# Kernel optimization log

Hardware: AMD Instinct MI355X
Metric: run time of the kernel (lower is better)

The kernel has to match this reference:

```python
import jax, jax.numpy as jnp
import numpy as np

N_VALUES = 10
STRIDE = 2

# sign binarization with straight-through estimator (identity gradient)
@jax.custom_vjp
def binarize(x):
    return jnp.sign(x)

def _bin_fwd(x):
    return jnp.sign(x), None

def _bin_bwd(res, g):
    return (g,)

binarize.defvjp(_bin_fwd, _bin_bwd)


def setup_inputs() -> dict:
    key = jax.random.key(0)
    k1, k2, k3, k4 = jax.random.split(key, 4)
    B, C, H = 16, 1, 28
    D = 2048
    x = jax.random.uniform(k1, (B, C, H, H), dtype=jnp.float32)          # float image in [0,1)
    values = jax.random.normal(k2, (N_VALUES, D), dtype=jnp.float32)     # value-vector embedding table
    w = jax.random.normal(k3, (D, D, 5, 5), dtype=jnp.float32) * 0.05    # binary conv weight (OIHW)
    b = jax.random.normal(k4, (D,), dtype=jnp.float32) * 0.01            # conv bias
    return {"x": x, "values": values, "w": w, "b": b}


def reference(x, values, w, b):
    n = values.shape[0]
    # quantize pixel intensities to value-vector indices (truncation, like .long())
    idx = (x[:, 0] * (n - 1)).astype(jnp.int32)            # [B, H, W]
    # embedding lookup of binarized value vectors
    emb = binarize(values)[idx]                            # [B, H, W, D]
    emb = jnp.transpose(emb, (0, 3, 1, 2))                 # [B, D, H, W]
    # binary-weight conv2d, kernel 5, stride 2, no padding
    out = jax.lax.conv_general_dilated(
        emb, binarize(w),
        window_strides=(STRIDE, STRIDE), padding='VALID',
        dimension_numbers=('NCHW', 'OIHW', 'NCHW'))
    out = out + b[None, :, None, None]                     # [B, D, 12, 12]
    return binarize(out)
```

## Files before the change

### kernel.cpp

```cpp
#include <hip/hip_runtime.h>

#define NV    10
#define DD    2048
#define TAPS  25
#define CHUNK 128
#define NCH   (DD / CHUNK)
#define NGRP  (DD / 64)
#define OB    64

typedef __attribute__((address_space(1))) const unsigned int gu32;
typedef __attribute__((address_space(3))) unsigned int lu32;

__device__ __forceinline__ float bsign(float v) {
    return (v > 0.0f) ? 1.0f : ((v < 0.0f) ? -1.0f : 0.0f);
}


__global__ __launch_bounds__(64) void vpack_kernel(
        const float* __restrict__ values,
        unsigned long long* __restrict__ vnz,
        unsigned long long* __restrict__ vng) {
    const int b    = blockIdx.x;
    const int n    = b >> 5;
    const int g    = b & 31;
    const int lane = threadIdx.x;
    float f = values[n * DD + g * 64 + lane];
    unsigned long long nz = __ballot(f != 0.0f);
    unsigned long long ng = __ballot(f < 0.0f);
    if (lane == 0) {
        vnz[n * NGRP + g] = nz;
        vng[n * NGRP + g] = ng;
    }
}

__global__ __launch_bounds__(256) void g_kernel(
        const float* __restrict__ w,
        const unsigned long long* __restrict__ gvnz,
        const unsigned long long* __restrict__ gvng,
        float* __restrict__ G) {
    const int o    = blockIdx.x;
    const int t    = threadIdx.x;
    const int lane = t & 63;
    const int wv   = t >> 6;

    __shared__ float ls_raw[CHUNK * TAPS + 32];
    __shared__ unsigned long long s_wnz[TAPS * 2];
    __shared__ unsigned long long s_wng[TAPS * 2];
    __shared__ unsigned long long s_vnz[NV * NGRP];
    __shared__ unsigned long long s_vng[NV * NGRP];

    for (int e = t; e < NV * NGRP; e += 256) {
        s_vnz[e] = gvnz[e];
        s_vng[e] = gvng[e];
    }

    const int tap = t / NV;
    const int n   = t - tap * NV;
    int acc = 0;

    const float* wo = w + (size_t)o * (DD * TAPS);

    for (int ch = 0; ch < NCH; ++ch) {
        __syncthreads();
        const float* src = wo + (size_t)(ch * CHUNK) * TAPS;
        for (int e = t; e < (CHUNK * TAPS) / 4; e += 256) {
            const float* gp = src + 4 * e;
            float* lp = ls_raw + 4 * (e - lane);
            __builtin_amdgcn_global_load_lds((gu32*)gp, (lu32*)lp, 16, 0, 0);
        }
        __syncthreads();
        for (int task = wv; task < TAPS * 2; task += 4) {
            const int ptap = task >> 1;
            const int sub  = task & 1;
            float f = ls_raw[(sub * 64 + lane) * TAPS + ptap];
            unsigned long long nz = __ballot(f != 0.0f);
            unsigned long long ng = __ballot(f < 0.0f);
            if (lane == 0) { s_wnz[task] = nz; s_wng[task] = ng; }
        }
        __syncthreads();
        if (t < NV * TAPS) {
            #pragma unroll
            for (int sub = 0; sub < 2; ++sub) {
                unsigned long long wnz = s_wnz[tap * 2 + sub];
                unsigned long long wng = s_wng[tap * 2 + sub];
                unsigned long long vz  = s_vnz[n * NGRP + ch * 2 + sub];
                unsigned long long vg  = s_vng[n * NGRP + ch * 2 + sub];
                unsigned long long nzb = wnz & vz;
                unsigned long long df  = (wng ^ vg) & nzb;
                acc += __popcll(nzb) - 2 * __popcll(df);
            }
        }
    }
    if (t < NV * TAPS) {
        G[((size_t)(tap * NV + n) << 11) + o] = (float)acc;
    }
}

__global__ __launch_bounds__(256) void out_kernel(
        const float* __restrict__ x,
        const float* __restrict__ G,
        const float* __restrict__ bias,
        float* __restrict__ out) {
    const int b     = blockIdx.x >> 5;
    const int oc    = blockIdx.x & 31;
    const int obase = oc * OB;
    const int t     = threadIdx.x;
    const int lane  = t & 63;
    const int oq    = t >> 6;

    __shared__ float s_G[TAPS * NV * 65];
    __shared__ int   s_idx[28 * 28];
    __shared__ float s_bias[OB];

    for (int e = t; e < TAPS * NV * 16; e += 256) {
        const int r  = e >> 4;
        const int li = (e & 15) << 2;
        const float4 v = *(const float4*)(G + ((size_t)r << 11) + obase + li);
        s_G[r * 65 + li]     = v.x;
        s_G[r * 65 + li + 1] = v.y;
        s_G[r * 65 + li + 2] = v.z;
        s_G[r * 65 + li + 3] = v.w;
    }
    for (int e = t; e < 28 * 28; e += 256) {
        s_idx[e] = (int)(x[b * 784 + e] * 9.0f);
    }
    if (t < OB) s_bias[t] = bias[obase + t];
    __syncthreads();

    for (int grp = 0; grp < 3; ++grp) {
        const int pos = grp * 64 + lane;
        if (pos < 144) {
            const int oh = pos / 12;
            const int ow = pos - oh * 12;
            int rr[25];
            #pragma unroll
            for (int kh = 0; kh < 5; ++kh) {
                const int row = (oh * 2 + kh) * 28 + ow * 2;
                #pragma unroll
                for (int kw = 0; kw < 5; ++kw) {
                    const int nn = s_idx[row + kw];
                    rr[kh * 5 + kw] = (kh * 5 + kw) * 650 + nn * 65;
                }
            }
            for (int ol = oq; ol < OB; ol += 4) {
                float acc = 0.0f;
                #pragma unroll
                for (int tp = 0; tp < TAPS; ++tp) {
                    acc += s_G[rr[tp] + ol];
                }
                out[((size_t)(b * DD + obase + ol)) * 144 + pos] = bsign(acc + s_bias[ol]);
            }
        }
    }
}

extern "C" void kernel_launch(void* const* d_in, const int* in_sizes, int n_in,
                              void* d_out, int out_size, void* d_ws, size_t ws_size,
                              hipStream_t stream) {
    const float* x      = (const float*)d_in[0];
    const float* values = (const float*)d_in[1];
    const float* w      = (const float*)d_in[2];
    const float* bias   = (const float*)d_in[3];
    float* out = (float*)d_out;

    unsigned long long* vnz = (unsigned long long*)d_ws;
    unsigned long long* vng = vnz + NV * NGRP;
    float* G = (float*)((char*)d_ws + 8192);

    hipLaunchKernelGGL(vpack_kernel, dim3(NV * NGRP), dim3(64), 0, stream, values, vnz, vng);
    hipLaunchKernelGGL(g_kernel, dim3(DD), dim3(256), 0, stream, w, vnz, vng, G);
    hipLaunchKernelGGL(out_kernel, dim3(16 * (DD / OB)), dim3(256), 0, stream, x, G, bias, out);
}
```

Baseline: 123.8 us.

## Fuse value-vector packing into g_kernel and double-buffer weight sign masks

Drops the separate vpack_kernel launch: each g_kernel block now builds its own value-vector sign and nonzero bitmasks from the values table. The chunk loop is restructured so the next weight chunk's async global-to-LDS load is issued before the popcount work on the previous chunk's masks, which are double-buffered in shared memory. This removes one kernel launch and its dependency, and tries to overlap weight streaming with mask arithmetic. In exchange, every one of the 2048 blocks re-reads the full 80 KB values table, which adds a large amount of redundant L2 traffic to a kernel that is already bandwidth bound.

```diff
diff --git a/kernel.cpp b/kernel.cpp
--- a/kernel.cpp
+++ b/kernel.cpp
@@ -15,28 +15,9 @@
     return (v > 0.0f) ? 1.0f : ((v < 0.0f) ? -1.0f : 0.0f);
 }
 
-
-__global__ __launch_bounds__(64) void vpack_kernel(
+__global__ __launch_bounds__(256) void g_kernel(
         const float* __restrict__ values,
-        unsigned long long* __restrict__ vnz,
-        unsigned long long* __restrict__ vng) {
-    const int b    = blockIdx.x;
-    const int n    = b >> 5;
-    const int g    = b & 31;
-    const int lane = threadIdx.x;
-    float f = values[n * DD + g * 64 + lane];
-    unsigned long long nz = __ballot(f != 0.0f);
-    unsigned long long ng = __ballot(f < 0.0f);
-    if (lane == 0) {
-        vnz[n * NGRP + g] = nz;
-        vng[n * NGRP + g] = ng;
-    }
-}
-
-__global__ __launch_bounds__(256) void g_kernel(
         const float* __restrict__ w,
-        const unsigned long long* __restrict__ gvnz,
-        const unsigned long long* __restrict__ gvng,
         float* __restrict__ G) {
     const int o    = blockIdx.x;
     const int t    = threadIdx.x;
@@ -44,53 +25,74 @@
     const int wv   = t >> 6;
 
     __shared__ float ls_raw[CHUNK * TAPS + 32];
-    __shared__ unsigned long long s_wnz[TAPS * 2];
-    __shared__ unsigned long long s_wng[TAPS * 2];
+    __shared__ unsigned long long s_wnz[2][TAPS * 2];
+    __shared__ unsigned long long s_wng[2][TAPS * 2];
     __shared__ unsigned long long s_vnz[NV * NGRP];
     __shared__ unsigned long long s_vng[NV * NGRP];
 
-    for (int e = t; e < NV * NGRP; e += 256) {
-        s_vnz[e] = gvnz[e];
-        s_vng[e] = gvng[e];
+    const float* wo = w + (size_t)o * (DD * TAPS);
+
+    for (int e = t; e < (CHUNK * TAPS) / 4; e += 256) {
+        __builtin_amdgcn_global_load_lds((gu32*)(wo + 4 * e),
+                                         (lu32*)(ls_raw + 4 * (e - lane)), 16, 0, 0);
     }
+    for (int t2 = wv; t2 < NGRP * NV; t2 += 4) {
+        const int g = t2 / NV;
+        const int n = t2 - g * NV;
+        float f = values[n * DD + g * 64 + lane];
+        unsigned long long nz = __ballot(f != 0.0f);
+        unsigned long long ng = __ballot(f < 0.0f);
+        if (lane == 0) { s_vnz[n * NGRP + g] = nz; s_vng[n * NGRP + g] = ng; }
+    }
+    __syncthreads();
+    for (int task = wv; task < TAPS * 2; task += 4) {
+        const int ptap = task >> 1;
+        const int sub  = task & 1;
+        float f = ls_raw[(sub * 64 + lane) * TAPS + ptap];
+        unsigned long long nz = __ballot(f != 0.0f);
+        unsigned long long ng = __ballot(f < 0.0f);
+        if (lane == 0) { s_wnz[0][task] = nz; s_wng[0][task] = ng; }
+    }
+    __syncthreads();
 
     const int tap = t / NV;
     const int n   = t - tap * NV;
     int acc = 0;
 
-    const float* wo = w + (size_t)o * (DD * TAPS);
-
-    for (int ch = 0; ch < NCH; ++ch) {
-        __syncthreads();
-        const float* src = wo + (size_t)(ch * CHUNK) * TAPS;
-        for (int e = t; e < (CHUNK * TAPS) / 4; e += 256) {
-            const float* gp = src + 4 * e;
-            float* lp = ls_raw + 4 * (e - lane);
-            __builtin_amdgcn_global_load_lds((gu32*)gp, (lu32*)lp, 16, 0, 0);
+    for (int ch = 1; ch <= NCH; ++ch) {
+        if (ch < NCH) {
+            const float* src = wo + (size_t)(ch * CHUNK) * TAPS;
+            for (int e = t; e < (CHUNK * TAPS) / 4; e += 256) {
+                __builtin_amdgcn_global_load_lds((gu32*)(src + 4 * e),
+                                                 (lu32*)(ls_raw + 4 * (e - lane)), 16, 0, 0);
+            }
         }
-        __syncthreads();
-        for (int task = wv; task < TAPS * 2; task += 4) {
-            const int ptap = task >> 1;
-            const int sub  = task & 1;
-            float f = ls_raw[(sub * 64 + lane) * TAPS + ptap];
-            unsigned long long nz = __ballot(f != 0.0f);
-            unsigned long long ng = __ballot(f < 0.0f);
-            if (lane == 0) { s_wnz[task] = nz; s_wng[task] = ng; }
-        }
-        __syncthreads();
         if (t < NV * TAPS) {
+            const int pb = (ch - 1) & 1;
             #pragma unroll
             for (int sub = 0; sub < 2; ++sub) {
-                unsigned long long wnz = s_wnz[tap * 2 + sub];
-                unsigned long long wng = s_wng[tap * 2 + sub];
-                unsigned long long vz  = s_vnz[n * NGRP + ch * 2 + sub];
-                unsigned long long vg  = s_vng[n * NGRP + ch * 2 + sub];
+                unsigned long long wnz = s_wnz[pb][tap * 2 + sub];
+                unsigned long long wng = s_wng[pb][tap * 2 + sub];
+                unsigned long long vz  = s_vnz[n * NGRP + (ch - 1) * 2 + sub];
+                unsigned long long vg  = s_vng[n * NGRP + (ch - 1) * 2 + sub];
                 unsigned long long nzb = wnz & vz;
-                unsigned long long df  = (wng ^ vg) & nzb;
-                acc += __popcll(nzb) - 2 * __popcll(df);
+                acc += (int)__popcll(nzb) - 2 * (int)__popcll((wng ^ vg) & nzb);
             }
         }
+        if (ch < NCH) {
+            __syncthreads();
+            for (int task = wv; task < TAPS * 2; task += 4) {
+                const int ptap = task >> 1;
+                const int sub  = task & 1;
+                float f = ls_raw[(sub * 64 + lane) * TAPS + ptap];
+                unsigned long long nz = __ballot(f != 0.0f);
+                unsigned long long ng = __ballot(f < 0.0f);
+                if (lane == 0) { s_wnz[ch & 1][task] = nz; s_wng[ch & 1][task] = ng; }
+            }
+            __syncthreads();
+        }
     }
+
     if (t < NV * TAPS) {
         G[((size_t)(tap * NV + n) << 11) + o] = (float)acc;
     }
@@ -162,12 +164,8 @@
     const float* w      = (const float*)d_in[2];
     const float* bias   = (const float*)d_in[3];
     float* out = (float*)d_out;
+    float* G   = (float*)d_ws;
 
-    unsigned long long* vnz = (unsigned long long*)d_ws;
-    unsigned long long* vng = vnz + NV * NGRP;
-    float* G = (float*)((char*)d_ws + 8192);
-
-    hipLaunchKernelGGL(vpack_kernel, dim3(NV * NGRP), dim3(64), 0, stream, values, vnz, vng);
-    hipLaunchKernelGGL(g_kernel, dim3(DD), dim3(256), 0, stream, w, vnz, vng, G);
+    hipLaunchKernelGGL(g_kernel, dim3(DD), dim3(256), 0, stream, values, w, G);
     hipLaunchKernelGGL(out_kernel, dim3(16 * (DD / OB)), dim3(256), 0, stream, x, G, bias, out);
 }
```

After: 151.5 us. +22.4%, slower.
